# Kernel optimization log

Hardware: AMD Instinct MI355X
Metric: run time of the kernel (lower is better)

The kernel has to match this reference:

```python
import jax, jax.numpy as jnp
import numpy as np

B, K, D = 4096, 16, 256
NUM_CODES = 512
BETA = 0.25  # commitment (activation_entropy=None path)
LN_EPS = 1e-5

def setup_inputs() -> dict:
    key = jax.random.key(0)
    ks = jax.random.split(key, 6)
    hidden = jax.random.normal(ks[0], (B, K, D), dtype=jnp.float32)
    active_mask = jax.random.randint(ks[1], (B, K), 0, 2).astype(bool)
    bound = 1.0 / NUM_CODES
    codebook = jax.random.uniform(ks[2], (NUM_CODES, D), minval=-bound, maxval=bound, dtype=jnp.float32)
    lim = 1.0 / np.sqrt(D)
    W_in = jax.random.uniform(ks[3], (D, D), minval=-lim, maxval=lim, dtype=jnp.float32)
    W_out = jax.random.uniform(ks[4], (D, D), minval=-lim, maxval=lim, dtype=jnp.float32)
    ln_gamma = jnp.ones((D,), jnp.float32)
    ln_beta = jnp.zeros((D,), jnp.float32)
    return {"hidden": hidden, "active_mask": active_mask, "codebook": codebook,
            "W_in": W_in, "W_out": W_out, "ln_gamma": ln_gamma, "ln_beta": ln_beta}

def reference(hidden, active_mask, codebook, W_in, W_out, ln_gamma, ln_beta):
    sg = jax.lax.stop_gradient
    z = jnp.einsum('bkd,ed->bke', hidden, W_in)              # proj_in (no bias)
    z_flat = z.reshape(-1, D)                                 # [B*K, D]
    # ||z - c||^2 = |z|^2 - 2 z.c + |c|^2
    dist = (jnp.sum(z_flat * z_flat, -1, keepdims=True)
            - 2.0 * z_flat @ codebook.T
            + jnp.sum(codebook * codebook, -1))               # [B*K, C]
    idx = jnp.argmin(dist, axis=-1)                           # [B*K]
    z_q = codebook[idx].reshape(z.shape)                      # gather
    vq_loss = jnp.mean((sg(z_q) - z) ** 2) + BETA * jnp.mean((z_q - sg(z)) ** 2)
    z_st = z + sg(z_q - z)                                    # straight-through
    out = jnp.einsum('bkd,ed->bke', z_st, W_out)              # proj_out
    h = hidden + active_mask[..., None].astype(jnp.float32) * out
    mu = jnp.mean(h, -1, keepdims=True)
    var = jnp.mean((h - mu) ** 2, -1, keepdims=True)
    h_comm = (h - mu) * jax.lax.rsqrt(var + LN_EPS) * ln_gamma + ln_beta
    return h_comm, vq_loss
```

## Files before the change

### kernel.cpp

```cpp
#include <hip/hip_runtime.h>
#include <hip/hip_bf16.h>

#define RTOT  65536
#define DDIM  256
#define NCODE 512
#define LN_EPS 1e-5f

typedef short bf16x8 __attribute__((ext_vector_type(8)));
typedef float f32x4  __attribute__((ext_vector_type(4)));

__device__ __forceinline__ unsigned short f2bf(float f) {
  unsigned u = __float_as_uint(f);
  u += 0x7fffu + ((u >> 16) & 1u);
  return (unsigned short)(u >> 16);
}
__device__ __forceinline__ float bf2f(unsigned short s) {
  return __uint_as_float(((unsigned)s) << 16);
}

__global__ __launch_bounds__(256) void prep_kernel(
    const float* __restrict__ codebook, const float* __restrict__ W_in,
    const float* __restrict__ W_out,
    float* __restrict__ loss_acc, float* __restrict__ c2,
    float* __restrict__ code_out, unsigned short* __restrict__ Wb,
    unsigned short* __restrict__ CBb) {
  __shared__ float ws4[4];
  __shared__ float cbl[256];
  const int b = blockIdx.x, t = threadIdx.x;
  if (b < 256) {
    int i = b * 256 + t;
    Wb[i] = f2bf(W_in[i]);
  } else if (b < 768) {
    int c = b - 256;
    float v = codebook[c * 256 + t];
    CBb[c * 256 + t] = f2bf(v);
    float sq = v * v;
    #pragma unroll
    for (int m = 1; m < 64; m <<= 1) sq += __shfl_xor(sq, m);
    if ((t & 63) == 0) ws4[t >> 6] = sq;
    __syncthreads();
    if (t == 0) {
      c2[c] = ws4[0] + ws4[1] + ws4[2] + ws4[3];
      if (c == 0) *loss_acc = 0.f;
    }
  } else {
    int c = b - 768;
    cbl[t] = codebook[c * 256 + t];
    __syncthreads();
    const float* wrow = W_out + t * 256;
    float acc = 0.f;
    #pragma unroll 4
    for (int d = 0; d < 256; d += 4) {
      float4 w = *(const float4*)(wrow + d);
      acc += cbl[d] * w.x + cbl[d+1] * w.y + cbl[d+2] * w.z + cbl[d+3] * w.w;
    }
    code_out[c * 256 + t] = acc;
  }
}

__global__ __launch_bounds__(256, 2) void main_kernel(
    const float* __restrict__ hidden, const int* __restrict__ mask,
    const float* __restrict__ gamma, const float* __restrict__ beta,
    const float* __restrict__ c2g, const float* __restrict__ code_out,
    const unsigned short* __restrict__ Wb, const unsigned short* __restrict__ CBb,
    float* __restrict__ loss_acc, float* __restrict__ out) {

  __shared__ union {
    struct { unsigned short A[64 * 40]; unsigned short Bw[256 * 40]; } p1;
    unsigned short CB[256 * 40];
  } st;
  __shared__ unsigned short Z[64 * 264];
  __shared__ float z2[64];
  __shared__ float c2s[512];
  __shared__ float sminv[4 * 64];
  __shared__ int   sminc[4 * 64];
  __shared__ int   ridx[64];

  const int t    = threadIdx.x;
  const int lane = t & 63;
  const int w    = t >> 6;
  const int l15  = lane & 15;
  const int quad = lane >> 4;
  const int row0 = blockIdx.x * 64;

  c2s[t]       = c2g[t];
  c2s[t + 256] = c2g[t + 256];

  const f32x4 zf = {0.f, 0.f, 0.f, 0.f};

  f32x4 acc1[4][4];
  #pragma unroll
  for (int i = 0; i < 4; i++)
    #pragma unroll
    for (int j = 0; j < 4; j++) acc1[i][j] = zf;

  const int arow = t >> 2;
  const int akq  = t & 3;
  const float* hsrc = hidden + (size_t)(row0 + arow) * 256 + akq * 8;
  unsigned short* Ast = st.p1.A + arow * 40 + akq * 8;

  for (int ks = 0; ks < 8; ks++) {
    {
      const float4* p = (const float4*)(hsrc + ks * 32);
      float4 x0 = p[0], x1 = p[1];
      bf16x8 v;
      v[0] = (short)f2bf(x0.x); v[1] = (short)f2bf(x0.y);
      v[2] = (short)f2bf(x0.z); v[3] = (short)f2bf(x0.w);
      v[4] = (short)f2bf(x1.x); v[5] = (short)f2bf(x1.y);
      v[6] = (short)f2bf(x1.z); v[7] = (short)f2bf(x1.w);
      *(bf16x8*)Ast = v;
    }
    #pragma unroll
    for (int it = 0; it < 4; it++) {
      int idx = t + it * 256;
      int rrow = idx >> 2, kq = idx & 3;
      bf16x8 v = *(const bf16x8*)(Wb + rrow * 256 + ks * 32 + kq * 8);
      *(bf16x8*)(st.p1.Bw + rrow * 40 + kq * 8) = v;
    }
    __syncthreads();
    bf16x8 a[4];
    #pragma unroll
    for (int i = 0; i < 4; i++)
      a[i] = *(const bf16x8*)(st.p1.A + (i * 16 + l15) * 40 + quad * 8);
    #pragma unroll
    for (int j = 0; j < 4; j++) {
      bf16x8 bb = *(const bf16x8*)(st.p1.Bw + (w * 64 + j * 16 + l15) * 40 + quad * 8);
      #pragma unroll
      for (int i = 0; i < 4; i++)
        acc1[i][j] = __builtin_amdgcn_mfma_f32_16x16x32_bf16(a[i], bb, acc1[i][j], 0, 0, 0);
    }
    __syncthreads();
  }

  #pragma unroll
  for (int i = 0; i < 4; i++)
    #pragma unroll
    for (int j = 0; j < 4; j++)
      #pragma unroll
      for (int r = 0; r < 4; r++) {
        int zr = i * 16 + quad * 4 + r;
        int zc = w * 64 + j * 16 + l15;
        Z[zr * 264 + zc] = f2bf(acc1[i][j][r]);
      }
  __syncthreads();

  {
    int zr = t >> 2, part = t & 3;
    float s = 0.f;
    const unsigned short* zp = Z + zr * 264 + part * 64;
    #pragma unroll
    for (int c = 0; c < 64; c += 8) {
      bf16x8 v = *(const bf16x8*)(zp + c);
      #pragma unroll
      for (int e = 0; e < 8; e++) { float f = bf2f((unsigned short)v[e]); s += f * f; }
    }
    s += __shfl_xor(s, 1);
    s += __shfl_xor(s, 2);
    if (part == 0) z2[zr] = s;
  }
  __syncthreads();

  float runv[16];
  int   runc[16];
  #pragma unroll
  for (int r = 0; r < 16; r++) { runv[r] = 3.4e38f; runc[r] = 0; }

  for (int pass = 0; pass < 2; pass++) {
    f32x4 acc2[4][4];
    #pragma unroll
    for (int i = 0; i < 4; i++)
      #pragma unroll
      for (int j = 0; j < 4; j++) acc2[i][j] = zf;

    for (int ks = 0; ks < 8; ks++) {
      #pragma unroll
      for (int it = 0; it < 4; it++) {
        int idx = t + it * 256;
        int rrow = idx >> 2, kq = idx & 3;
        bf16x8 v = *(const bf16x8*)(CBb + (pass * 256 + rrow) * 256 + ks * 32 + kq * 8);
        *(bf16x8*)(st.CB + rrow * 40 + kq * 8) = v;
      }
      __syncthreads();
      bf16x8 a[4];
      #pragma unroll
      for (int i = 0; i < 4; i++)
        a[i] = *(const bf16x8*)(Z + (i * 16 + l15) * 264 + ks * 32 + quad * 8);
      #pragma unroll
      for (int j = 0; j < 4; j++) {
        bf16x8 bb = *(const bf16x8*)(st.CB + (w * 64 + j * 16 + l15) * 40 + quad * 8);
        #pragma unroll
        for (int i = 0; i < 4; i++)
          acc2[i][j] = __builtin_amdgcn_mfma_f32_16x16x32_bf16(a[i], bb, acc2[i][j], 0, 0, 0);
      }
      __syncthreads();
    }
    #pragma unroll
    for (int i = 0; i < 4; i++)
      #pragma unroll
      for (int j = 0; j < 4; j++) {
        int code = pass * 256 + w * 64 + j * 16 + l15;
        float cc = c2s[code];
        #pragma unroll
        for (int r = 0; r < 4; r++) {
          float s = cc - 2.f * acc2[i][j][r];
          int ri = i * 4 + r;
          if (s < runv[ri]) { runv[ri] = s; runc[ri] = code; }
        }
      }
  }

  #pragma unroll
  for (int ri = 0; ri < 16; ri++) {
    float v = runv[ri]; int c = runc[ri];
    #pragma unroll
    for (int m = 1; m < 16; m <<= 1) {
      float ov = __shfl_xor(v, m);
      int   oc = __shfl_xor(c, m);
      if (ov < v || (ov == v && oc < c)) { v = ov; c = oc; }
    }
    if (l15 == 0) {
      int i = ri >> 2, r = ri & 3;
      int row = i * 16 + quad * 4 + r;
      sminv[w * 64 + row] = v;
      sminc[w * 64 + row] = c;
    }
  }
  __syncthreads();

  if (t < 64) {
    int row = t;
    float bv = sminv[row]; int bc = sminc[row];
    #pragma unroll
    for (int ww = 1; ww < 4; ww++) {
      float v = sminv[ww * 64 + row]; int c = sminc[ww * 64 + row];
      if (v < bv || (v == bv && c < bc)) { bv = v; bc = c; }
    }
    ridx[row] = bc;
    float dist = z2[row] + bv;
    #pragma unroll
    for (int m = 1; m < 64; m <<= 1) dist += __shfl_xor(dist, m);
    if (t == 0) atomicAdd(loss_acc, dist);
  }
  __syncthreads();

  {
    float4 g4 = *(const float4*)(gamma + lane * 4);
    float4 b4 = *(const float4*)(beta + lane * 4);
    for (int rr = 0; rr < 16; rr++) {
      int row = w * 16 + rr;
      int gr  = row0 + row;
      float4 h = *(const float4*)(hidden + (size_t)gr * 256 + lane * 4);
      int code = ridx[row];
      float4 o = *(const float4*)(code_out + code * 256 + lane * 4);
      float mf = mask[gr] ? 1.f : 0.f;
      h.x += mf * o.x; h.y += mf * o.y; h.z += mf * o.z; h.w += mf * o.w;
      float s  = h.x + h.y + h.z + h.w;
      float sq = h.x * h.x + h.y * h.y + h.z * h.z + h.w * h.w;
      #pragma unroll
      for (int m = 1; m < 64; m <<= 1) { s += __shfl_xor(s, m); sq += __shfl_xor(sq, m); }
      float mean = s * (1.f / 256.f);
      float var  = sq * (1.f / 256.f) - mean * mean;
      float rstd = rsqrtf(var + LN_EPS);
      float4 res;
      res.x = (h.x - mean) * rstd * g4.x + b4.x;
      res.y = (h.y - mean) * rstd * g4.y + b4.y;
      res.z = (h.z - mean) * rstd * g4.z + b4.z;
      res.w = (h.w - mean) * rstd * g4.w + b4.w;
      *(float4*)(out + (size_t)gr * 256 + lane * 4) = res;
    }
  }
}

__global__ void loss_kernel(const float* __restrict__ loss_acc, float* __restrict__ out) {
  out[16777216] = 1.25f * loss_acc[0] * (1.f / 16777216.f);
}

extern "C" void kernel_launch(void* const* d_in, const int* in_sizes, int n_in,
                              void* d_out, int out_size, void* d_ws, size_t ws_size,
                              hipStream_t stream) {
  (void)in_sizes; (void)n_in; (void)out_size; (void)ws_size;
  const float* hidden   = (const float*)d_in[0];
  const int*   mask     = (const int*)d_in[1];
  const float* codebook = (const float*)d_in[2];
  const float* W_in     = (const float*)d_in[3];
  const float* W_out    = (const float*)d_in[4];
  const float* gamma    = (const float*)d_in[5];
  const float* beta     = (const float*)d_in[6];
  float* out = (float*)d_out;

  float* wsf      = (float*)d_ws;
  float* loss_acc = wsf;
  float* c2       = wsf + 64;
  float* code_out = wsf + 64 + 512;
  unsigned short* Wb  = (unsigned short*)(wsf + 64 + 512 + 512 * 256);
  unsigned short* CBb = Wb + 256 * 256;

  prep_kernel<<<1280, 256, 0, stream>>>(codebook, W_in, W_out, loss_acc, c2, code_out, Wb, CBb);
  main_kernel<<<1024, 256, 0, stream>>>(hidden, mask, gamma, beta, c2, code_out, Wb, CBb, loss_acc, out);
  loss_kernel<<<1, 1, 0, stream>>>(loss_acc, out);
}
```

Baseline: 203.4 us.

## Pipeline weight/codebook chunks via async LDS loads and fuse loss finalization

Prep now writes W_in and the codebook as 24 pre-tiled, XOR-swizzled bf16 chunks, so the main kernel can stream them with direct global-to-LDS loads into a double buffer. It also stages the whole hidden tile to LDS as bf16 once, and runs proj_in plus both codebook passes as one 24-chunk loop. The separate loss kernel is replaced by a last-block ticket inside the main kernel, and the code_out matmul in prep is tiled through shared memory. The goal is to hide global load latency, remove per-step barriers and bank conflicts, and drop one launch. The cost is more complex synchronization and larger LDS use, which may lower occupancy.

```diff
diff --git a/kernel.cpp b/kernel.cpp
--- a/kernel.cpp
+++ b/kernel.cpp
@@ -1,9 +1,5 @@
 #include <hip/hip_runtime.h>
-#include <hip/hip_bf16.h>
-
-#define RTOT  65536
-#define DDIM  256
-#define NCODE 512
+
 #define LN_EPS 1e-5f
 
 typedef short bf16x8 __attribute__((ext_vector_type(8)));
@@ -17,44 +13,81 @@
 __device__ __forceinline__ float bf2f(unsigned short s) {
   return __uint_as_float(((unsigned)s) << 16);
 }
+__device__ __forceinline__ int swz(int r) { return (r ^ (r >> 2)) & 3; }
+
+__device__ __forceinline__ bf16x8 pack8(float4 a, float4 b) {
+  bf16x8 v;
+  v[0] = (short)f2bf(a.x); v[1] = (short)f2bf(a.y);
+  v[2] = (short)f2bf(a.z); v[3] = (short)f2bf(a.w);
+  v[4] = (short)f2bf(b.x); v[5] = (short)f2bf(b.y);
+  v[6] = (short)f2bf(b.z); v[7] = (short)f2bf(b.w);
+  return v;
+}
+
+__device__ __forceinline__ void ldst16(const unsigned short* g, unsigned short* l) {
+  __builtin_amdgcn_global_load_lds(
+      (const __attribute__((address_space(1))) unsigned int*)g,
+      (__attribute__((address_space(3))) unsigned int*)l, 16, 0, 0);
+}
 
 __global__ __launch_bounds__(256) void prep_kernel(
     const float* __restrict__ codebook, const float* __restrict__ W_in,
     const float* __restrict__ W_out,
-    float* __restrict__ loss_acc, float* __restrict__ c2,
-    float* __restrict__ code_out, unsigned short* __restrict__ Wb,
-    unsigned short* __restrict__ CBb) {
-  __shared__ float ws4[4];
-  __shared__ float cbl[256];
+    float* __restrict__ loss_acc, unsigned* __restrict__ ticket,
+    float* __restrict__ c2, float* __restrict__ code_out,
+    unsigned short* __restrict__ BT) {
   const int b = blockIdx.x, t = threadIdx.x;
-  if (b < 256) {
-    int i = b * 256 + t;
-    Wb[i] = f2bf(W_in[i]);
-  } else if (b < 768) {
-    int c = b - 256;
-    float v = codebook[c * 256 + t];
-    CBb[c * 256 + t] = f2bf(v);
-    float sq = v * v;
-    #pragma unroll
-    for (int m = 1; m < 64; m <<= 1) sq += __shfl_xor(sq, m);
-    if ((t & 63) == 0) ws4[t >> 6] = sq;
+  if (b < 32) {
+    if (b == 0 && t == 0) { *loss_acc = 0.f; *ticket = 0u; }
+    int e = b * 8 + (t >> 5);
+    int c32 = t & 31, ks = c32 >> 2, kq = c32 & 3;
+    const float* src = W_in + e * 256 + c32 * 8;
+    float4 x0 = *(const float4*)src, x1 = *(const float4*)(src + 4);
+    *(bf16x8*)(BT + ks * 8192 + e * 32 + ((kq ^ swz(e)) * 8)) = pack8(x0, x1);
+  } else if (b < 96) {
+    int code = (b - 32) * 8 + (t >> 5);
+    int c32 = t & 31, ks = c32 >> 2, kq = c32 & 3;
+    const float* src = codebook + code * 256 + c32 * 8;
+    float4 x0 = *(const float4*)src, x1 = *(const float4*)(src + 4);
+    int rl = code & 255;
+    int chunk = 8 + (code >> 8) * 8 + ks;
+    *(bf16x8*)(BT + chunk * 8192 + rl * 32 + ((kq ^ swz(rl)) * 8)) = pack8(x0, x1);
+    float s = x0.x * x0.x + x0.y * x0.y + x0.z * x0.z + x0.w * x0.w +
+              x1.x * x1.x + x1.y * x1.y + x1.z * x1.z + x1.w * x1.w;
+    s += __shfl_xor(s, 1);  s += __shfl_xor(s, 2);
+    s += __shfl_xor(s, 4);  s += __shfl_xor(s, 8);
+    s += __shfl_xor(s, 16);
+    if ((t & 31) == 0) c2[code] = s;
+  } else {
+    __shared__ float Cs[32][260];
+    __shared__ float Ws[16][260];
+    int bi = b - 96, ci = bi & 15, ei = bi >> 4;
+    {
+      int row = t >> 4, col = (t & 15) * 16;
+      const float4* s = (const float4*)(W_out + (size_t)(ei * 16 + row) * 256 + col);
+      float4* d = (float4*)&Ws[row][col];
+      d[0] = s[0]; d[1] = s[1]; d[2] = s[2]; d[3] = s[3];
+    }
+    {
+      int row = t >> 3, col = (t & 7) * 32;
+      const float4* s = (const float4*)(codebook + (size_t)(ci * 32 + row) * 256 + col);
+      float4* d = (float4*)&Cs[row][col];
+      #pragma unroll
+      for (int k = 0; k < 8; k++) d[k] = s[k];
+    }
     __syncthreads();
-    if (t == 0) {
-      c2[c] = ws4[0] + ws4[1] + ws4[2] + ws4[3];
-      if (c == 0) *loss_acc = 0.f;
-    }
-  } else {
-    int c = b - 768;
-    cbl[t] = codebook[c * 256 + t];
-    __syncthreads();
-    const float* wrow = W_out + t * 256;
-    float acc = 0.f;
+    int c = t & 31, e0 = t >> 5;
+    float a0 = 0.f, a1 = 0.f;
     #pragma unroll 4
     for (int d = 0; d < 256; d += 4) {
-      float4 w = *(const float4*)(wrow + d);
-      acc += cbl[d] * w.x + cbl[d+1] * w.y + cbl[d+2] * w.z + cbl[d+3] * w.w;
-    }
-    code_out[c * 256 + t] = acc;
+      float4 cv = *(const float4*)&Cs[c][d];
+      float4 w0 = *(const float4*)&Ws[e0][d];
+      float4 w1 = *(const float4*)&Ws[e0 + 8][d];
+      a0 += cv.x * w0.x + cv.y * w0.y + cv.z * w0.z + cv.w * w0.w;
+      a1 += cv.x * w1.x + cv.y * w1.y + cv.z * w1.z + cv.w * w1.w;
+    }
+    code_out[(size_t)(ci * 32 + c) * 256 + ei * 16 + e0]     = a0;
+    code_out[(size_t)(ci * 32 + c) * 256 + ei * 16 + e0 + 8] = a1;
   }
 }
 
@@ -62,18 +95,16 @@
     const float* __restrict__ hidden, const int* __restrict__ mask,
     const float* __restrict__ gamma, const float* __restrict__ beta,
     const float* __restrict__ c2g, const float* __restrict__ code_out,
-    const unsigned short* __restrict__ Wb, const unsigned short* __restrict__ CBb,
-    float* __restrict__ loss_acc, float* __restrict__ out) {
-
-  __shared__ union {
-    struct { unsigned short A[64 * 40]; unsigned short Bw[256 * 40]; } p1;
-    unsigned short CB[256 * 40];
-  } st;
-  __shared__ unsigned short Z[64 * 264];
+    const unsigned short* __restrict__ BT,
+    float* __restrict__ loss_acc, unsigned* __restrict__ ticket,
+    float* __restrict__ out) {
+
+  __shared__ unsigned short HZ[64 * 264];
+  __shared__ unsigned short Bbuf[2][8192];
+  __shared__ float c2s[512];
   __shared__ float z2[64];
-  __shared__ float c2s[512];
-  __shared__ float sminv[4 * 64];
-  __shared__ int   sminc[4 * 64];
+  __shared__ float sminv[256];
+  __shared__ int   sminc[256];
   __shared__ int   ridx[64];
 
   const int t    = threadIdx.x;
@@ -86,127 +117,117 @@
   c2s[t]       = c2g[t];
   c2s[t + 256] = c2g[t + 256];
 
+  {
+    int r = t >> 2, q4 = t & 3;
+    const float* src = hidden + (size_t)(row0 + r) * 256 + q4 * 64;
+    unsigned short* dst = HZ + r * 264 + q4 * 64;
+    #pragma unroll
+    for (int j = 0; j < 8; j++) {
+      float4 x0 = *(const float4*)(src + j * 8);
+      float4 x1 = *(const float4*)(src + j * 8 + 4);
+      *(bf16x8*)(dst + j * 8) = pack8(x0, x1);
+    }
+  }
+  __syncthreads();
+
   const f32x4 zf = {0.f, 0.f, 0.f, 0.f};
-
-  f32x4 acc1[4][4];
+  f32x4 acc[4][4];
   #pragma unroll
   for (int i = 0; i < 4; i++)
     #pragma unroll
-    for (int j = 0; j < 4; j++) acc1[i][j] = zf;
-
-  const int arow = t >> 2;
-  const int akq  = t & 3;
-  const float* hsrc = hidden + (size_t)(row0 + arow) * 256 + akq * 8;
-  unsigned short* Ast = st.p1.A + arow * 40 + akq * 8;
-
-  for (int ks = 0; ks < 8; ks++) {
-    {
-      const float4* p = (const float4*)(hsrc + ks * 32);
-      float4 x0 = p[0], x1 = p[1];
-      bf16x8 v;
-      v[0] = (short)f2bf(x0.x); v[1] = (short)f2bf(x0.y);
-      v[2] = (short)f2bf(x0.z); v[3] = (short)f2bf(x0.w);
-      v[4] = (short)f2bf(x1.x); v[5] = (short)f2bf(x1.y);
-      v[6] = (short)f2bf(x1.z); v[7] = (short)f2bf(x1.w);
-      *(bf16x8*)Ast = v;
-    }
-    #pragma unroll
-    for (int it = 0; it < 4; it++) {
-      int idx = t + it * 256;
-      int rrow = idx >> 2, kq = idx & 3;
-      bf16x8 v = *(const bf16x8*)(Wb + rrow * 256 + ks * 32 + kq * 8);
-      *(bf16x8*)(st.p1.Bw + rrow * 40 + kq * 8) = v;
-    }
-    __syncthreads();
-    bf16x8 a[4];
-    #pragma unroll
-    for (int i = 0; i < 4; i++)
-      a[i] = *(const bf16x8*)(st.p1.A + (i * 16 + l15) * 40 + quad * 8);
-    #pragma unroll
-    for (int j = 0; j < 4; j++) {
-      bf16x8 bb = *(const bf16x8*)(st.p1.Bw + (w * 64 + j * 16 + l15) * 40 + quad * 8);
-      #pragma unroll
-      for (int i = 0; i < 4; i++)
-        acc1[i][j] = __builtin_amdgcn_mfma_f32_16x16x32_bf16(a[i], bb, acc1[i][j], 0, 0, 0);
-    }
-    __syncthreads();
-  }
-
-  #pragma unroll
-  for (int i = 0; i < 4; i++)
-    #pragma unroll
-    for (int j = 0; j < 4; j++)
-      #pragma unroll
-      for (int r = 0; r < 4; r++) {
-        int zr = i * 16 + quad * 4 + r;
-        int zc = w * 64 + j * 16 + l15;
-        Z[zr * 264 + zc] = f2bf(acc1[i][j][r]);
-      }
-  __syncthreads();
-
-  {
-    int zr = t >> 2, part = t & 3;
-    float s = 0.f;
-    const unsigned short* zp = Z + zr * 264 + part * 64;
-    #pragma unroll
-    for (int c = 0; c < 64; c += 8) {
-      bf16x8 v = *(const bf16x8*)(zp + c);
-      #pragma unroll
-      for (int e = 0; e < 8; e++) { float f = bf2f((unsigned short)v[e]); s += f * f; }
-    }
-    s += __shfl_xor(s, 1);
-    s += __shfl_xor(s, 2);
-    if (part == 0) z2[zr] = s;
-  }
-  __syncthreads();
+    for (int j = 0; j < 4; j++) acc[i][j] = zf;
 
   float runv[16];
   int   runc[16];
   #pragma unroll
   for (int r = 0; r < 16; r++) { runv[r] = 3.4e38f; runc[r] = 0; }
 
-  for (int pass = 0; pass < 2; pass++) {
-    f32x4 acc2[4][4];
+  {
+    const unsigned short* g = BT + w * 2048 + lane * 8;
+    unsigned short* l = &Bbuf[0][w * 2048];
+    #pragma unroll
+    for (int q = 0; q < 4; q++) ldst16(g + q * 512, l + q * 512);
+  }
+
+  for (int chunk = 0; chunk < 24; chunk++) {
+    const int cu = chunk & 1;
+    if (chunk == 8) {
+      __builtin_amdgcn_s_waitcnt(0x0F70);
+      __syncthreads();
+      #pragma unroll
+      for (int i = 0; i < 4; i++)
+        #pragma unroll
+        for (int j = 0; j < 4; j++)
+          #pragma unroll
+          for (int r = 0; r < 4; r++)
+            HZ[(i * 16 + quad * 4 + r) * 264 + (w * 64 + j * 16 + l15)] =
+                f2bf(acc[i][j][r]);
+      __syncthreads();
+      {
+        int zr = t >> 2, part = t & 3;
+        float s = 0.f;
+        const unsigned short* zp = HZ + zr * 264 + part * 64;
+        #pragma unroll
+        for (int c = 0; c < 64; c += 8) {
+          bf16x8 v = *(const bf16x8*)(zp + c);
+          #pragma unroll
+          for (int e = 0; e < 8; e++) { float f = bf2f((unsigned short)v[e]); s += f * f; }
+        }
+        s += __shfl_xor(s, 1);
+        s += __shfl_xor(s, 2);
+        if (part == 0) z2[zr] = s;
+      }
+      #pragma unroll
+      for (int i = 0; i < 4; i++)
+        #pragma unroll
+        for (int j = 0; j < 4; j++) acc[i][j] = zf;
+    } else {
+      __builtin_amdgcn_s_waitcnt(0x0F70);
+    }
+
+    if (chunk < 23) {
+      const unsigned short* g = BT + (chunk + 1) * 8192 + w * 2048 + lane * 8;
+      unsigned short* l = &Bbuf[cu ^ 1][w * 2048];
+      #pragma unroll
+      for (int q = 0; q < 4; q++) ldst16(g + q * 512, l + q * 512);
+    }
+
+    const int ks = chunk & 7;
+    bf16x8 a[4];
     #pragma unroll
     for (int i = 0; i < 4; i++)
-      #pragma unroll
-      for (int j = 0; j < 4; j++) acc2[i][j] = zf;
-
-    for (int ks = 0; ks < 8; ks++) {
-      #pragma unroll
-      for (int it = 0; it < 4; it++) {
-        int idx = t + it * 256;
-        int rrow = idx >> 2, kq = idx & 3;
-        bf16x8 v = *(const bf16x8*)(CBb + (pass * 256 + rrow) * 256 + ks * 32 + kq * 8);
-        *(bf16x8*)(st.CB + rrow * 40 + kq * 8) = v;
+      a[i] = *(const bf16x8*)(HZ + (i * 16 + l15) * 264 + ks * 32 + quad * 8);
+    #pragma unroll
+    for (int j = 0; j < 4; j++) {
+      int c = w * 64 + j * 16 + l15;
+      bf16x8 bb = *(const bf16x8*)(&Bbuf[cu][c * 32 + ((quad ^ swz(c)) * 8)]);
+      #pragma unroll
+      for (int i = 0; i < 4; i++)
+        acc[i][j] = __builtin_amdgcn_mfma_f32_16x16x32_bf16(a[i], bb, acc[i][j], 0, 0, 0);
+    }
+
+    if (chunk == 15 || chunk == 23) {
+      int pass = (chunk - 8) >> 3;
+      #pragma unroll
+      for (int i = 0; i < 4; i++)
+        #pragma unroll
+        for (int j = 0; j < 4; j++) {
+          int code = pass * 256 + w * 64 + j * 16 + l15;
+          float cc = c2s[code];
+          #pragma unroll
+          for (int r = 0; r < 4; r++) {
+            float s = cc - 2.f * acc[i][j][r];
+            int ri = i * 4 + r;
+            if (s < runv[ri]) { runv[ri] = s; runc[ri] = code; }
+          }
+        }
+      if (chunk == 15) {
+        #pragma unroll
+        for (int i = 0; i < 4; i++)
+          #pragma unroll
+          for (int j = 0; j < 4; j++) acc[i][j] = zf;
       }
-      __syncthreads();
-      bf16x8 a[4];
-      #pragma unroll
-      for (int i = 0; i < 4; i++)
-        a[i] = *(const bf16x8*)(Z + (i * 16 + l15) * 264 + ks * 32 + quad * 8);
-      #pragma unroll
-      for (int j = 0; j < 4; j++) {
-        bf16x8 bb = *(const bf16x8*)(st.CB + (w * 64 + j * 16 + l15) * 40 + quad * 8);
-        #pragma unroll
-        for (int i = 0; i < 4; i++)
-          acc2[i][j] = __builtin_amdgcn_mfma_f32_16x16x32_bf16(a[i], bb, acc2[i][j], 0, 0, 0);
-      }
-      __syncthreads();
-    }
-    #pragma unroll
-    for (int i = 0; i < 4; i++)
-      #pragma unroll
-      for (int j = 0; j < 4; j++) {
-        int code = pass * 256 + w * 64 + j * 16 + l15;
-        float cc = c2s[code];
-        #pragma unroll
-        for (int r = 0; r < 4; r++) {
-          float s = cc - 2.f * acc2[i][j][r];
-          int ri = i * 4 + r;
-          if (s < runv[ri]) { runv[ri] = s; runc[ri] = code; }
-        }
-      }
+    }
   }
 
   #pragma unroll
@@ -239,7 +260,15 @@
     float dist = z2[row] + bv;
     #pragma unroll
     for (int m = 1; m < 64; m <<= 1) dist += __shfl_xor(dist, m);
-    if (t == 0) atomicAdd(loss_acc, dist);
+    if (t == 0) {
+      atomicAdd(loss_acc, dist);
+      __threadfence();
+      unsigned done = atomicAdd(ticket, 1u);
+      if (done == gridDim.x - 1) {
+        float total = atomicAdd(loss_acc, 0.f);
+        out[16777216] = 1.25f * total * (1.f / 16777216.f);
+      }
+    }
   }
   __syncthreads();
 
@@ -251,7 +280,7 @@
       int gr  = row0 + row;
       float4 h = *(const float4*)(hidden + (size_t)gr * 256 + lane * 4);
       int code = ridx[row];
-      float4 o = *(const float4*)(code_out + code * 256 + lane * 4);
+      float4 o = *(const float4*)(code_out + (size_t)code * 256 + lane * 4);
       float mf = mask[gr] ? 1.f : 0.f;
       h.x += mf * o.x; h.y += mf * o.y; h.z += mf * o.z; h.w += mf * o.w;
       float s  = h.x + h.y + h.z + h.w;
@@ -269,10 +298,6 @@
       *(float4*)(out + (size_t)gr * 256 + lane * 4) = res;
     }
   }
-}
-
-__global__ void loss_kernel(const float* __restrict__ loss_acc, float* __restrict__ out) {
-  out[16777216] = 1.25f * loss_acc[0] * (1.f / 16777216.f);
 }
 
 extern "C" void kernel_launch(void* const* d_in, const int* in_sizes, int n_in,
@@ -290,12 +315,13 @@
 
   float* wsf      = (float*)d_ws;
   float* loss_acc = wsf;
+  unsigned* ticket = (unsigned*)(wsf + 1);
   float* c2       = wsf + 64;
   float* code_out = wsf + 64 + 512;
-  unsigned short* Wb  = (unsigned short*)(wsf + 64 + 512 + 512 * 256);
-  unsigned short* CBb = Wb + 256 * 256;
-
-  prep_kernel<<<1280, 256, 0, stream>>>(codebook, W_in, W_out, loss_acc, c2, code_out, Wb, CBb);
-  main_kernel<<<1024, 256, 0, stream>>>(hidden, mask, gamma, beta, c2, code_out, Wb, CBb, loss_acc, out);
-  loss_kernel<<<1, 1, 0, stream>>>(loss_acc, out);
-}
+  unsigned short* BT = (unsigned short*)(wsf + 64 + 512 + 512 * 256);
+
+  prep_kernel<<<352, 256, 0, stream>>>(codebook, W_in, W_out, loss_acc, ticket,
+                                       c2, code_out, BT);
+  main_kernel<<<1024, 256, 0, stream>>>(hidden, mask, gamma, beta, c2, code_out,
+                                        BT, loss_acc, ticket, out);
+}
```

Result: slower. 209.5 us (+3.0%).
